# Optimization experiments

Hardware: AMD Instinct MI355X
Metric: run time of the kernel (lower is better)

Reference implementation:

```python
import jax, jax.numpy as jnp
import numpy as np

B, S, E, HEADS, LATENT = 8, 4096, 2048, 16, 64
HEAD_SIZE = E // HEADS  # 128
NEG = -1e20


def setup_inputs() -> dict:
    key = jax.random.key(0)
    k0, k1, k2, k3, k4 = jax.random.split(key, 5)
    return {
        "x": jax.random.normal(k0, (B, S, E), dtype=jnp.float32) * 0.02,
        "W_dkv": jax.random.normal(k1, (LATENT, E), dtype=jnp.float32) * 0.02,
        "W_k": jax.random.normal(k2, (HEAD_SIZE, LATENT), dtype=jnp.float32) * 0.02,
        "W_v": jax.random.normal(k3, (HEAD_SIZE, LATENT), dtype=jnp.float32) * 0.02,
        "W_q": jax.random.normal(k4, (HEAD_SIZE, E), dtype=jnp.float32) * 0.02,
    }


def reference(x, W_dkv, W_k, W_v, W_q):
    # x: [B,S,E]; nn.Linear computes x @ W.T (weight layout [out,in])
    head_size = W_k.shape[0]
    latent = jnp.einsum("bse,le->bsl", x, W_dkv)        # latent KV cache [B,S,L]
    absorbed_q = W_q.T @ W_k                              # [E,H] @ [H,L] -> [E,L]
    q_res = jnp.einsum("bse,el->bsl", x, absorbed_q)     # [B,S,L]
    scale = head_size ** -0.5
    scores = jnp.einsum("bql,bkl->bqk", q_res, latent) * scale  # [B,S,S]
    seq = x.shape[1]
    causal = jnp.tril(jnp.ones((seq, seq), dtype=bool))
    scores = jnp.where(causal, scores, NEG)
    attn = jax.nn.softmax(scores, axis=-1)               # dropout skipped (eval mode)
    v = jnp.einsum("bsl,hl->bsh", latent, W_v)           # compressed V [B,S,H]
    out = jnp.einsum("bqk,bkh->bqh", attn, v)            # [B,S,head_size]
    return out, latent  # latent == kv_cache returned by the module
```

## Files before the change

kernel.cpp:

```cpp
#include <hip/hip_runtime.h>
#include <hip/hip_bf16.h>

#define NB 8
#define NS 4096
#define NE 2048
#define NL 64
#define NH 128
#define NM (NB*NS)

typedef unsigned short ushort_t;
typedef __attribute__((ext_vector_type(4))) float f32x4;
typedef __attribute__((ext_vector_type(8))) __bf16 bf16x8;
typedef __attribute__((ext_vector_type(8))) unsigned short u16x8;
typedef __attribute__((ext_vector_type(4))) unsigned short u16x4;

#define SCALE2 0.1275174537f

__device__ __forceinline__ float fast_exp2(float x) {
    return __builtin_amdgcn_exp2f(x);
}

__device__ __forceinline__ unsigned short f2bf(float f) {
    union { float f; unsigned u; } v; v.f = f;
    unsigned u = v.u + 0x7fffu + ((v.u >> 16) & 1u);
    return (unsigned short)(u >> 16);
}

__device__ __forceinline__ float bf2f(ushort_t u) {
    union { unsigned u; float f; } v; v.u = (unsigned)u << 16; return v.f;
}

__device__ __forceinline__ int swz(int row, int colbyte) {
    return (row * 128 + colbyte) ^ ((row & 7) << 4);
}

__device__ __forceinline__ void wg_barrier() {
    asm volatile("s_waitcnt lgkmcnt(0)" ::: "memory");
    __builtin_amdgcn_s_barrier();
    __builtin_amdgcn_sched_barrier(0);
}

__global__ __launch_bounds__(256) void prep_kernel(
    const float* __restrict__ Wdkv, const float* __restrict__ Wk,
    const float* __restrict__ Wq, ushort_t* __restrict__ WcatT)
{
    __shared__ float wk[128 * 64];
    const int t = threadIdx.x;
    for (int i = t; i < 128 * 64; i += 256) wk[i] = Wk[i];
    __syncthreads();
    const int e = blockIdx.x * 256 + t;
    const int l0 = blockIdx.y * 16;
    float acc[16];
    #pragma unroll
    for (int l = 0; l < 16; ++l) acc[l] = 0.f;
    for (int h = 0; h < 128; ++h) {
        float q = Wq[h * NE + e];
        #pragma unroll
        for (int l = 0; l < 16; ++l) acc[l] += q * wk[h * 64 + l0 + l];
    }
    for (int l = 0; l < 16; ++l) WcatT[(64 + l0 + l) * NE + e] = f2bf(acc[l] * SCALE2);
    for (int l = 0; l < 16; ++l) WcatT[(l0 + l) * NE + e] = f2bf(Wdkv[(l0 + l) * NE + e]);
}

__global__ __launch_bounds__(256) void proj_kernel(
    const float* __restrict__ x, const ushort_t* __restrict__ WcatT,
    float* __restrict__ latent_out, ushort_t* __restrict__ k_bf,
    ushort_t* __restrict__ q_bf, ushort_t* __restrict__ kt)
{
    __shared__ ushort_t As[2][64 * 64];
    __shared__ ushort_t Bs[2][128 * 64];
    const int tid = threadIdx.x;
    const int w = tid >> 6, lane = tid & 63, lg = lane >> 4, li = lane & 15;
    const int m0 = blockIdx.x * 64;
    const int wm = (w >> 1) * 32, wn = (w & 1) * 64;
    const int srow = tid >> 3, scol = tid & 7;

    f32x4 acc[2][4];
    #pragma unroll
    for (int i = 0; i < 2; ++i)
        #pragma unroll
        for (int j = 0; j < 4; ++j) acc[i][j] = f32x4{0.f, 0.f, 0.f, 0.f};

    f32x4 a0reg[2][2], a1reg[2][2];
    u16x8 b0reg[4], b1reg[4];

#define PLOAD(k0, AR, BR) do { \
    _Pragma("unroll") for (int p = 0; p < 2; ++p) { \
        const float* gp = x + (long)(m0 + srow + 32 * p) * NE + (k0) + scol * 8; \
        AR[p][0] = *reinterpret_cast<const f32x4*>(gp); \
        AR[p][1] = *reinterpret_cast<const f32x4*>(gp + 4); } \
    _Pragma("unroll") for (int p = 0; p < 4; ++p) \
        BR[p] = *reinterpret_cast<const u16x8*>(WcatT + (long)(srow + 32 * p) * NE + (k0) + scol * 8); \
} while (0)

#define PWRITE(AR, BR, buf) do { \
    _Pragma("unroll") for (int p = 0; p < 2; ++p) { \
        union { unsigned uw[4]; u16x8 v; } hu; \
        asm("v_cvt_pk_bf16_f32 %0, %1, %2" : "=v"(hu.uw[0]) : "v"(AR[p][0][0]), "v"(AR[p][0][1])); \
        asm("v_cvt_pk_bf16_f32 %0, %1, %2" : "=v"(hu.uw[1]) : "v"(AR[p][0][2]), "v"(AR[p][0][3])); \
        asm("v_cvt_pk_bf16_f32 %0, %1, %2" : "=v"(hu.uw[2]) : "v"(AR[p][1][0]), "v"(AR[p][1][1])); \
        asm("v_cvt_pk_bf16_f32 %0, %1, %2" : "=v"(hu.uw[3]) : "v"(AR[p][1][2]), "v"(AR[p][1][3])); \
        *reinterpret_cast<u16x8*>(reinterpret_cast<char*>(As[buf]) + swz(srow + 32 * p, scol * 16)) = hu.v; } \
    _Pragma("unroll") for (int p = 0; p < 4; ++p) \
        *reinterpret_cast<u16x8*>(reinterpret_cast<char*>(Bs[buf]) + swz(srow + 32 * p, scol * 16)) = BR[p]; \
} while (0)

    auto compute = [&](int buf) {
        #pragma unroll
        for (int c = 0; c < 2; ++c) {
            bf16x8 af[2], bfv[4];
            #pragma unroll
            for (int mf = 0; mf < 2; ++mf)
                af[mf] = *reinterpret_cast<const bf16x8*>(
                    reinterpret_cast<const char*>(As[buf]) + swz(wm + 16 * mf + li, c * 64 + lg * 16));
            #pragma unroll
            for (int nf = 0; nf < 4; ++nf)
                bfv[nf] = *reinterpret_cast<const bf16x8*>(
                    reinterpret_cast<const char*>(Bs[buf]) + swz(wn + 16 * nf + li, c * 64 + lg * 16));
            #pragma unroll
            for (int mf = 0; mf < 2; ++mf)
                #pragma unroll
                for (int nf = 0; nf < 4; ++nf)
                    acc[mf][nf] = __builtin_amdgcn_mfma_f32_16x16x32_bf16(
                        af[mf], bfv[nf], acc[mf][nf], 0, 0, 0);
        }
    };

    PLOAD(0, a0reg, b0reg);
    PLOAD(64, a1reg, b1reg);
    PWRITE(a0reg, b0reg, 0);
    wg_barrier();

    for (int ks = 0; ks < 32; ks += 2) {
        if (ks + 2 < 32) PLOAD((ks + 2) * 64, a0reg, b0reg);
        compute(0);
        PWRITE(a1reg, b1reg, 1);
        wg_barrier();
        if (ks + 3 < 32) PLOAD((ks + 3) * 64, a1reg, b1reg);
        compute(1);
        if (ks + 2 < 32) PWRITE(a0reg, b0reg, 0);
        wg_barrier();
    }

    const int b = m0 >> 12, s0 = m0 & 4095;
    #pragma unroll
    for (int mf = 0; mf < 2; ++mf) {
        #pragma unroll
        for (int nf = 0; nf < 4; ++nf) {
            int col = wn + 16 * nf + li;
            #pragma unroll
            for (int r = 0; r < 4; ++r) {
                int row = m0 + wm + 16 * mf + 4 * lg + r;
                float v = acc[mf][nf][r];
                if (wn == 0) {
                    latent_out[(long)row * NL + col] = v;
                    k_bf[(long)row * NL + col] = f2bf(v);
                    *reinterpret_cast<ushort_t*>(reinterpret_cast<char*>(As[0]) +
                        swz(wm + 16 * mf + 4 * lg + r, col * 2)) = f2bf(v);
                } else {
                    q_bf[(long)row * NL + (col - 64)] = f2bf(v);
                }
            }
        }
    }
    wg_barrier();
    union { u16x8 u; bf16x8 v; } iu;
    #pragma unroll
    for (int j = 0; j < 8; ++j)
        iu.u[j] = (lg == (li >> 3) + 2 * (w & 1) && (li & 7) == j)
                      ? (ushort_t)0x3F80 : (ushort_t)0;
    const int ckt = w >> 1;
    f32x4 ktacc[4];
    #pragma unroll
    for (int nf = 0; nf < 4; ++nf) {
        bf16x8 bfv = *reinterpret_cast<const bf16x8*>(
            reinterpret_cast<const char*>(As[0]) + swz(16 * nf + li, ckt * 64 + lg * 16));
        ktacc[nf] = __builtin_amdgcn_mfma_f32_16x16x32_bf16(
            iu.v, bfv, f32x4{0.f, 0.f, 0.f, 0.f}, 0, 0, 0);
    }
    #pragma unroll
    for (int nf = 0; nf < 4; ++nf)
        #pragma unroll
        for (int r = 0; r < 4; ++r)
            kt[(long)(b * 64 + 16 * w + 4 * lg + r) * NS + s0 + 16 * nf + li] =
                f2bf(ktacc[nf][r]);
}

__global__ __launch_bounds__(256, 2) void attn_kernel(
    const ushort_t* __restrict__ q_bf, const ushort_t* __restrict__ k_bf,
    const ushort_t* __restrict__ kt, const float* __restrict__ Wv,
    float* __restrict__ out)
{
    __shared__ __attribute__((aligned(16))) char smem[34816];
    ushort_t* OW = (ushort_t*)smem;
    float* mw = (float*)(smem + 32768);
    float* lw = (float*)(smem + 33792);
    ushort_t* Ms = (ushort_t*)smem;
    ushort_t* Wvs = (ushort_t*)(smem + 8192);
    float* Os = (float*)smem;

    const int tid = threadIdx.x;
    const int w = tid >> 6, lane = tid & 63, lg = lane >> 4, li = lane & 15;
    const int l = blockIdx.x;
    const int b = l & 7;
    const int p_ = l >> 3;
    const int k_ = p_ >> 1, e_ = p_ & 1, kk = (k_ & 15) * 2;
    const int qt = (k_ >> 4) ? (e_ ? kk + 1 : 63 - kk) : (e_ ? 62 - kk : kk);
    const int Q0 = qt << 6;
    const int nch = (qt >> 1) + 1;

    const int krow = tid >> 1, khalf = tid & 1;
    const int trow = tid >> 2, tkq = (tid & 3) * 32;

    bf16x8 qf[4][2];
    #pragma unroll
    for (int qb = 0; qb < 4; ++qb)
        #pragma unroll
        for (int c = 0; c < 2; ++c)
            qf[qb][c] = *reinterpret_cast<const bf16x8*>(
                q_bf + ((long)b * NS + Q0 + 16 * qb + li) * NL + c * 32 + lg * 8);

    float m_r[4], l_r[4];
    #pragma unroll
    for (int qb = 0; qb < 4; ++qb) { m_r[qb] = -1.0e30f; l_r[qb] = 0.f; }
    f32x4 oacc[4][4];
    #pragma unroll
    for (int qb = 0; qb < 4; ++qb)
        #pragma unroll
        for (int n = 0; n < 4; ++n) oacc[qb][n] = f32x4{0.f, 0.f, 0.f, 0.f};

    u16x8 kreg[4], treg[4];

#define ALOAD(ch) do { \
    const int kv0_ = (ch) * 128; \
    _Pragma("unroll") for (int pp = 0; pp < 4; ++pp) \
        kreg[pp] = *reinterpret_cast<const u16x8*>( \
            k_bf + ((long)b * NS + kv0_ + krow) * NL + khalf * 32 + pp * 8); \
    _Pragma("unroll") for (int pp = 0; pp < 4; ++pp) \
        treg[pp] = *reinterpret_cast<const u16x8*>( \
            kt + ((long)b * 64 + trow) * NS + kv0_ + tkq + pp * 8); \
} while (0)

#define AWRITE() do { \
    char* Kb_ = smem; \
    char* Tb_ = smem + 16384; \
    _Pragma("unroll") for (int pp = 0; pp < 4; ++pp) \
        *reinterpret_cast<u16x8*>(Kb_ + swz(krow, khalf * 64 + pp * 16)) = kreg[pp]; \
    _Pragma("unroll") for (int pp = 0; pp < 4; ++pp) { \
        const int kv8 = tkq + pp * 8; \
        const int colp = (kv8 & 0x60) | ((kv8 & 0xC) << 1) | ((kv8 & 0x10) >> 2); \
        const int xo = (trow & 15) << 4; \
        u16x4 lo = {treg[pp][0], treg[pp][1], treg[pp][2], treg[pp][3]}; \
        u16x4 hi = {treg[pp][4], treg[pp][5], treg[pp][6], treg[pp][7]}; \
        *reinterpret_cast<u16x4*>(Tb_ + trow * 256 + ((colp * 2) ^ xo)) = lo; \
        *reinterpret_cast<u16x4*>(Tb_ + trow * 256 + (((colp + 8) * 2) ^ xo)) = hi; \
    } \
} while (0)

    auto compute = [&](bool diag, int kv0) {
        const char* Kb = smem;
        const char* Tb = smem + 16384;
        f32x4 s[2][4];
        #pragma unroll
        for (int kvb = 0; kvb < 2; ++kvb)
            #pragma unroll
            for (int qb = 0; qb < 4; ++qb) s[kvb][qb] = f32x4{0.f, 0.f, 0.f, 0.f};
        __builtin_amdgcn_s_setprio(1);
        #pragma unroll
        for (int c = 0; c < 2; ++c)
            #pragma unroll
            for (int kvb = 0; kvb < 2; ++kvb) {
                bf16x8 a = *reinterpret_cast<const bf16x8*>(
                    Kb + swz(32 * w + 16 * kvb + li, c * 64 + lg * 16));
                #pragma unroll
                for (int qb = 0; qb < 4; ++qb)
                    s[kvb][qb] = __builtin_amdgcn_mfma_f32_16x16x32_bf16(
                        a, qf[qb][c], s[kvb][qb], 0, 0, 0);
            }
        __builtin_amdgcn_s_setprio(0);
        if (diag) {
            #pragma unroll
            for (int kvb = 0; kvb < 2; ++kvb)
                #pragma unroll
                for (int qb = 0; qb < 4; ++qb)
                    #pragma unroll
                    for (int r = 0; r < 4; ++r) {
                        int kv_g = kv0 + 32 * w + 16 * kvb + 4 * lg + r;
                        int q_g = Q0 + 16 * qb + li;
                        if (kv_g > q_g) s[kvb][qb][r] = -3.0e38f;
                    }
        }
        float mx[4];
        #pragma unroll
        for (int qb = 0; qb < 4; ++qb) {
            float m0_ = fmaxf(fmaxf(s[0][qb][0], s[0][qb][1]), fmaxf(s[0][qb][2], s[0][qb][3]));
            float m1_ = fmaxf(fmaxf(s[1][qb][0], s[1][qb][1]), fmaxf(s[1][qb][2], s[1][qb][3]));
            mx[qb] = fmaxf(m0_, m1_);
        }
        bool ok = (mx[0] <= m_r[0] + 8.f) && (mx[1] <= m_r[1] + 8.f) &&
                  (mx[2] <= m_r[2] + 8.f) && (mx[3] <= m_r[3] + 8.f);
        if (!__all(ok)) {
            #pragma unroll
            for (int qb = 0; qb < 4; ++qb) {
                float mxf = fmaxf(mx[qb], __shfl_xor(mx[qb], 16));
                mxf = fmaxf(mxf, __shfl_xor(mxf, 32));
                float m_new = fmaxf(m_r[qb], mxf);
                float corr = fast_exp2(m_r[qb] - m_new);
                m_r[qb] = m_new;
                l_r[qb] *= corr;
                float corrO[4];
                #pragma unroll
                for (int r = 0; r < 4; ++r)
                    corrO[r] = __shfl(corr, (lane & 48) | (4 * lg + r));
                #pragma unroll
                for (int n = 0; n < 4; ++n)
                    #pragma unroll
                    for (int r = 0; r < 4; ++r) oacc[qb][n][r] *= corrO[r];
            }
        }
        #pragma unroll
        for (int qb = 0; qb < 4; ++qb) {
            float rs = 0.f;
            #pragma unroll
            for (int kvb = 0; kvb < 2; ++kvb)
                #pragma unroll
                for (int r = 0; r < 4; ++r) {
                    float pv = fast_exp2(s[kvb][qb][r] - m_r[qb]);
                    s[kvb][qb][r] = pv;
                    rs += pv;
                }
            l_r[qb] += rs;
        }
        bf16x8 vb[4];
        #pragma unroll
        for (int n = 0; n < 4; ++n)
            vb[n] = *reinterpret_cast<const bf16x8*>(
                Tb + (16 * n + li) * 256 + ((64 * w + 16 * lg) ^ (li << 4)));
        __builtin_amdgcn_s_setprio(1);
        #pragma unroll
        for (int qb = 0; qb < 4; ++qb) {
            union { unsigned uw[4]; bf16x8 v; } pa;
            asm("v_cvt_pk_bf16_f32 %0, %1, %2" : "=v"(pa.uw[0]) : "v"(s[0][qb][0]), "v"(s[0][qb][1]));
            asm("v_cvt_pk_bf16_f32 %0, %1, %2" : "=v"(pa.uw[1]) : "v"(s[0][qb][2]), "v"(s[0][qb][3]));
            asm("v_cvt_pk_bf16_f32 %0, %1, %2" : "=v"(pa.uw[2]) : "v"(s[1][qb][0]), "v"(s[1][qb][1]));
            asm("v_cvt_pk_bf16_f32 %0, %1, %2" : "=v"(pa.uw[3]) : "v"(s[1][qb][2]), "v"(s[1][qb][3]));
            #pragma unroll
            for (int n = 0; n < 4; ++n)
                oacc[qb][n] = __builtin_amdgcn_mfma_f32_16x16x32_bf16(
                    pa.v, vb[n], oacc[qb][n], 0, 0, 0);
        }
        __builtin_amdgcn_s_setprio(0);
    };

    ALOAD(0);
    AWRITE();
    wg_barrier();
    for (int i = 0; i < nch; ++i) {
        if (i + 1 < nch) ALOAD(i + 1);
        compute(i == nch - 1, i * 128);
        wg_barrier();
        if (i + 1 < nch) {
            AWRITE();
            wg_barrier();
        }
    }

    #pragma unroll
    for (int qb = 0; qb < 4; ++qb) {
        l_r[qb] += __shfl_xor(l_r[qb], 16);
        l_r[qb] += __shfl_xor(l_r[qb], 32);
    }
    if (lg == 0) {
        #pragma unroll
        for (int qb = 0; qb < 4; ++qb) {
            mw[w * 64 + 16 * qb + li] = m_r[qb];
            lw[w * 64 + 16 * qb + li] = l_r[qb];
        }
    }
    #pragma unroll
    for (int qb = 0; qb < 4; ++qb)
        #pragma unroll
        for (int r = 0; r < 4; ++r) {
            union { unsigned uw[2]; u16x4 v; } u;
            asm("v_cvt_pk_bf16_f32 %0, %1, %2" : "=v"(u.uw[0]) : "v"(oacc[qb][0][r]), "v"(oacc[qb][1][r]));
            asm("v_cvt_pk_bf16_f32 %0, %1, %2" : "=v"(u.uw[1]) : "v"(oacc[qb][2][r]), "v"(oacc[qb][3][r]));
            int q = 16 * qb + 4 * lg + r;
            *reinterpret_cast<u16x4*>(OW + (w * 64 + q) * 64 + li * 4) = u.v;
        }
    wg_barrier();

    float merged[16];
    {
        const int q = tid >> 2, g = tid & 3;
        float m4[4], l4[4];
        #pragma unroll
        for (int ww = 0; ww < 4; ++ww) { m4[ww] = mw[ww * 64 + q]; l4[ww] = lw[ww * 64 + q]; }
        float M = fmaxf(fmaxf(m4[0], m4[1]), fmaxf(m4[2], m4[3]));
        float cw[4], L = 0.f;
        #pragma unroll
        for (int ww = 0; ww < 4; ++ww) { cw[ww] = fast_exp2(m4[ww] - M); L += cw[ww] * l4[ww]; }
        float inv = 1.f / L;
        #pragma unroll
        for (int e = 0; e < 16; ++e) {
            float a = 0.f;
            #pragma unroll
            for (int ww = 0; ww < 4; ++ww)
                a += cw[ww] * bf2f(OW[(ww * 64 + q) * 64 + e * 4 + g]);
            merged[e] = a * inv;
        }
    }
    wg_barrier();

    {
        const int q = tid >> 2, g = tid & 3;
        #pragma unroll
        for (int ee = 0; ee < 8; ++ee) {
            unsigned pk;
            asm("v_cvt_pk_bf16_f32 %0, %1, %2" : "=v"(pk) : "v"(merged[2 * ee]), "v"(merged[2 * ee + 1]));
            *reinterpret_cast<unsigned*>(reinterpret_cast<char*>(Ms) + swz(q, g * 32 + 4 * ee)) = pk;
        }
        const int r = tid >> 1, hf = tid & 1;
        const float* wp = Wv + r * 64 + hf * 32;
        #pragma unroll
        for (int qq = 0; qq < 2; ++qq) {
            f32x4 w0 = *reinterpret_cast<const f32x4*>(wp + qq * 16);
            f32x4 w1 = *reinterpret_cast<const f32x4*>(wp + qq * 16 + 4);
            f32x4 w2 = *reinterpret_cast<const f32x4*>(wp + qq * 16 + 8);
            f32x4 w3 = *reinterpret_cast<const f32x4*>(wp + qq * 16 + 12);
            u16x8 h0, h1;
            #pragma unroll
            for (int jj = 0; jj < 4; ++jj) {
                h0[jj] = f2bf(w0[jj]); h0[4 + jj] = f2bf(w1[jj]);
                h1[jj] = f2bf(w2[jj]); h1[4 + jj] = f2bf(w3[jj]);
            }
            *reinterpret_cast<u16x8*>(reinterpret_cast<char*>(Wvs) + swz(r, hf * 64 + qq * 32)) = h0;
            *reinterpret_cast<u16x8*>(reinterpret_cast<char*>(Wvs) + swz(r, hf * 64 + qq * 32 + 16)) = h1;
        }
    }
    wg_barrier();

    f32x4 vacc[2][4];
    #pragma unroll
    for (int i = 0; i < 2; ++i)
        #pragma unroll
        for (int j = 0; j < 4; ++j) vacc[i][j] = f32x4{0.f, 0.f, 0.f, 0.f};
    #pragma unroll
    for (int c = 0; c < 2; ++c) {
        bf16x8 af[2], bfv[4];
        #pragma unroll
        for (int mf = 0; mf < 2; ++mf)
            af[mf] = *reinterpret_cast<const bf16x8*>(
                reinterpret_cast<const char*>(Wvs) + swz(32 * w + 16 * mf + li, c * 64 + lg * 16));
        #pragma unroll
        for (int nf = 0; nf < 4; ++nf)
            bfv[nf] = *reinterpret_cast<const bf16x8*>(
                reinterpret_cast<const char*>(Ms) + swz(16 * nf + li, c * 64 + lg * 16));
        #pragma unroll
        for (int mf = 0; mf < 2; ++mf)
            #pragma unroll
            for (int nf = 0; nf < 4; ++nf)
                vacc[mf][nf] = __builtin_amdgcn_mfma_f32_16x16x32_bf16(
                    af[mf], bfv[nf], vacc[mf][nf], 0, 0, 0);
    }
    wg_barrier();
    #pragma unroll
    for (int mf = 0; mf < 2; ++mf)
        #pragma unroll
        for (int nf = 0; nf < 4; ++nf)
            #pragma unroll
            for (int r = 0; r < 4; ++r)
                Os[(16 * nf + li) * 132 + 32 * w + 16 * mf + 4 * lg + r] = vacc[mf][nf][r];
    wg_barrier();
    {
        const int r = tid >> 2, cb = (tid & 3) * 32;
        float* op = out + ((long)b * NS + Q0 + r) * NH + cb;
        const float* sp = Os + r * 132 + cb;
        #pragma unroll
        for (int qq = 0; qq < 8; ++qq)
            *reinterpret_cast<f32x4*>(op + 4 * qq) = *reinterpret_cast<const f32x4*>(sp + 4 * qq);
    }
}

extern "C" void kernel_launch(void* const* d_in, const int* in_sizes, int n_in,
                              void* d_out, int out_size, void* d_ws, size_t ws_size,
                              hipStream_t stream) {
    const float* x    = (const float*)d_in[0];
    const float* Wdkv = (const float*)d_in[1];
    const float* Wk   = (const float*)d_in[2];
    const float* Wv   = (const float*)d_in[3];
    const float* Wq   = (const float*)d_in[4];

    float* out = (float*)d_out;
    float* latent_out = out + (long)NM * NH;

    ushort_t* WcatT = (ushort_t*)d_ws;
    ushort_t* q_bf  = WcatT + 128 * NE;
    ushort_t* k_bf  = q_bf + (long)NM * NL;
    ushort_t* kt    = k_bf + (long)NM * NL;

    hipLaunchKernelGGL(prep_kernel, dim3(NE / 256, 4), dim3(256), 0, stream, Wdkv, Wk, Wq, WcatT);
    hipLaunchKernelGGL(proj_kernel, dim3(NM / 64), dim3(256), 0, stream,
                       x, WcatT, latent_out, k_bf, q_bf, kt);
    hipLaunchKernelGGL(attn_kernel, dim3(512), dim3(256), 0, stream,
                       q_bf, k_bf, kt, Wv, out);
}
```

Before: 131.8 us.

## Halve attention query tile to 32 rows and double the grid

The attention kernel now processes 32 query rows per workgroup instead of 64 and launches 1024 workgroups instead of 512, with a new causal tile ordering that pairs short and long tiles. The aim is better CU occupancy and load balance on the 256-CU part, along with lower register pressure per block. The cross-wave merge is rewritten to use 8 threads per query row, a swizzled bf16 shared-memory layout and vectorized reads. In exchange, K/V tiles are reloaded from global/L2 twice as often per query, and each MFMA now has less reuse of the loaded K data.

```diff
diff --git a/kernel.cpp b/kernel.cpp
--- a/kernel.cpp
+++ b/kernel.cpp
@@ -194,38 +194,38 @@
     __shared__ __attribute__((aligned(16))) char smem[34816];
     ushort_t* OW = (ushort_t*)smem;
     float* mw = (float*)(smem + 32768);
-    float* lw = (float*)(smem + 33792);
+    float* lw = (float*)(smem + 33280);
     ushort_t* Ms = (ushort_t*)smem;
-    ushort_t* Wvs = (ushort_t*)(smem + 8192);
+    ushort_t* Wvs = (ushort_t*)(smem + 4096);
     float* Os = (float*)smem;
 
     const int tid = threadIdx.x;
     const int w = tid >> 6, lane = tid & 63, lg = lane >> 4, li = lane & 15;
-    const int l = blockIdx.x;
-    const int b = l & 7;
-    const int p_ = l >> 3;
-    const int k_ = p_ >> 1, e_ = p_ & 1, kk = (k_ & 15) * 2;
-    const int qt = (k_ >> 4) ? (e_ ? kk + 1 : 63 - kk) : (e_ ? 62 - kk : kk);
-    const int Q0 = qt << 6;
-    const int nch = (qt >> 1) + 1;
+    const int j = blockIdx.x;
+    const int b = j & 7;
+    const int s_ = j >> 3;
+    const int u_ = s_ & 63, e_ = s_ >> 6;
+    const int t = e_ ? u_ : 127 - u_;
+    const int Q0 = t << 5;
+    const int nch = (t >> 2) + 1;
 
     const int krow = tid >> 1, khalf = tid & 1;
     const int trow = tid >> 2, tkq = (tid & 3) * 32;
 
-    bf16x8 qf[4][2];
-    #pragma unroll
-    for (int qb = 0; qb < 4; ++qb)
+    bf16x8 qf[2][2];
+    #pragma unroll
+    for (int qb = 0; qb < 2; ++qb)
         #pragma unroll
         for (int c = 0; c < 2; ++c)
             qf[qb][c] = *reinterpret_cast<const bf16x8*>(
                 q_bf + ((long)b * NS + Q0 + 16 * qb + li) * NL + c * 32 + lg * 8);
 
-    float m_r[4], l_r[4];
-    #pragma unroll
-    for (int qb = 0; qb < 4; ++qb) { m_r[qb] = -1.0e30f; l_r[qb] = 0.f; }
-    f32x4 oacc[4][4];
-    #pragma unroll
-    for (int qb = 0; qb < 4; ++qb)
+    float m_r[2], l_r[2];
+    m_r[0] = m_r[1] = -1.0e30f;
+    l_r[0] = l_r[1] = 0.f;
+    f32x4 oacc[2][4];
+    #pragma unroll
+    for (int qb = 0; qb < 2; ++qb)
         #pragma unroll
         for (int n = 0; n < 4; ++n) oacc[qb][n] = f32x4{0.f, 0.f, 0.f, 0.f};
 
@@ -260,11 +260,11 @@
     auto compute = [&](bool diag, int kv0) {
         const char* Kb = smem;
         const char* Tb = smem + 16384;
-        f32x4 s[2][4];
+        f32x4 s[2][2];
         #pragma unroll
         for (int kvb = 0; kvb < 2; ++kvb)
             #pragma unroll
-            for (int qb = 0; qb < 4; ++qb) s[kvb][qb] = f32x4{0.f, 0.f, 0.f, 0.f};
+            for (int qb = 0; qb < 2; ++qb) s[kvb][qb] = f32x4{0.f, 0.f, 0.f, 0.f};
         __builtin_amdgcn_s_setprio(1);
         #pragma unroll
         for (int c = 0; c < 2; ++c)
@@ -273,7 +273,7 @@
                 bf16x8 a = *reinterpret_cast<const bf16x8*>(
                     Kb + swz(32 * w + 16 * kvb + li, c * 64 + lg * 16));
                 #pragma unroll
-                for (int qb = 0; qb < 4; ++qb)
+                for (int qb = 0; qb < 2; ++qb)
                     s[kvb][qb] = __builtin_amdgcn_mfma_f32_16x16x32_bf16(
                         a, qf[qb][c], s[kvb][qb], 0, 0, 0);
             }
@@ -282,7 +282,7 @@
             #pragma unroll
             for (int kvb = 0; kvb < 2; ++kvb)
                 #pragma unroll
-                for (int qb = 0; qb < 4; ++qb)
+                for (int qb = 0; qb < 2; ++qb)
                     #pragma unroll
                     for (int r = 0; r < 4; ++r) {
                         int kv_g = kv0 + 32 * w + 16 * kvb + 4 * lg + r;
@@ -290,18 +290,17 @@
                         if (kv_g > q_g) s[kvb][qb][r] = -3.0e38f;
                     }
         }
-        float mx[4];
-        #pragma unroll
-        for (int qb = 0; qb < 4; ++qb) {
+        float mx[2];
+        #pragma unroll
+        for (int qb = 0; qb < 2; ++qb) {
             float m0_ = fmaxf(fmaxf(s[0][qb][0], s[0][qb][1]), fmaxf(s[0][qb][2], s[0][qb][3]));
             float m1_ = fmaxf(fmaxf(s[1][qb][0], s[1][qb][1]), fmaxf(s[1][qb][2], s[1][qb][3]));
             mx[qb] = fmaxf(m0_, m1_);
         }
-        bool ok = (mx[0] <= m_r[0] + 8.f) && (mx[1] <= m_r[1] + 8.f) &&
-                  (mx[2] <= m_r[2] + 8.f) && (mx[3] <= m_r[3] + 8.f);
+        bool ok = (mx[0] <= m_r[0] + 8.f) && (mx[1] <= m_r[1] + 8.f);
         if (!__all(ok)) {
             #pragma unroll
-            for (int qb = 0; qb < 4; ++qb) {
+            for (int qb = 0; qb < 2; ++qb) {
                 float mxf = fmaxf(mx[qb], __shfl_xor(mx[qb], 16));
                 mxf = fmaxf(mxf, __shfl_xor(mxf, 32));
                 float m_new = fmaxf(m_r[qb], mxf);
@@ -319,7 +318,7 @@
             }
         }
         #pragma unroll
-        for (int qb = 0; qb < 4; ++qb) {
+        for (int qb = 0; qb < 2; ++qb) {
             float rs = 0.f;
             #pragma unroll
             for (int kvb = 0; kvb < 2; ++kvb)
@@ -338,7 +337,7 @@
                 Tb + (16 * n + li) * 256 + ((64 * w + 16 * lg) ^ (li << 4)));
         __builtin_amdgcn_s_setprio(1);
         #pragma unroll
-        for (int qb = 0; qb < 4; ++qb) {
+        for (int qb = 0; qb < 2; ++qb) {
             union { unsigned uw[4]; bf16x8 v; } pa;
             asm("v_cvt_pk_bf16_f32 %0, %1, %2" : "=v"(pa.uw[0]) : "v"(s[0][qb][0]), "v"(s[0][qb][1]));
             asm("v_cvt_pk_bf16_f32 %0, %1, %2" : "=v"(pa.uw[1]) : "v"(s[0][qb][2]), "v"(s[0][qb][3]));
@@ -366,58 +365,60 @@
     }
 
     #pragma unroll
-    for (int qb = 0; qb < 4; ++qb) {
+    for (int qb = 0; qb < 2; ++qb) {
         l_r[qb] += __shfl_xor(l_r[qb], 16);
         l_r[qb] += __shfl_xor(l_r[qb], 32);
     }
     if (lg == 0) {
         #pragma unroll
-        for (int qb = 0; qb < 4; ++qb) {
-            mw[w * 64 + 16 * qb + li] = m_r[qb];
-            lw[w * 64 + 16 * qb + li] = l_r[qb];
-        }
-    }
-    #pragma unroll
-    for (int qb = 0; qb < 4; ++qb)
+        for (int qb = 0; qb < 2; ++qb) {
+            mw[w * 32 + 16 * qb + li] = m_r[qb];
+            lw[w * 32 + 16 * qb + li] = l_r[qb];
+        }
+    }
+    #pragma unroll
+    for (int qb = 0; qb < 2; ++qb)
         #pragma unroll
         for (int r = 0; r < 4; ++r) {
             union { unsigned uw[2]; u16x4 v; } u;
             asm("v_cvt_pk_bf16_f32 %0, %1, %2" : "=v"(u.uw[0]) : "v"(oacc[qb][0][r]), "v"(oacc[qb][1][r]));
             asm("v_cvt_pk_bf16_f32 %0, %1, %2" : "=v"(u.uw[1]) : "v"(oacc[qb][2][r]), "v"(oacc[qb][3][r]));
             int q = 16 * qb + 4 * lg + r;
-            *reinterpret_cast<u16x4*>(OW + (w * 64 + q) * 64 + li * 4) = u.v;
-        }
-    wg_barrier();
-
-    float merged[16];
+            *reinterpret_cast<u16x4*>(smem + (w * 32 + q) * 128 + ((li * 8) ^ ((q & 7) << 4))) = u.v;
+        }
+    wg_barrier();
+
+    float acc8[8];
     {
-        const int q = tid >> 2, g = tid & 3;
+        const int q2 = tid >> 3, g = tid & 7;
         float m4[4], l4[4];
         #pragma unroll
-        for (int ww = 0; ww < 4; ++ww) { m4[ww] = mw[ww * 64 + q]; l4[ww] = lw[ww * 64 + q]; }
+        for (int ww = 0; ww < 4; ++ww) { m4[ww] = mw[ww * 32 + q2]; l4[ww] = lw[ww * 32 + q2]; }
         float M = fmaxf(fmaxf(m4[0], m4[1]), fmaxf(m4[2], m4[3]));
-        float cw[4], L = 0.f;
-        #pragma unroll
-        for (int ww = 0; ww < 4; ++ww) { cw[ww] = fast_exp2(m4[ww] - M); L += cw[ww] * l4[ww]; }
+        float a4[4], L = 0.f;
+        #pragma unroll
+        for (int ww = 0; ww < 4; ++ww) { a4[ww] = fast_exp2(m4[ww] - M); L += a4[ww] * l4[ww]; }
         float inv = 1.f / L;
         #pragma unroll
-        for (int e = 0; e < 16; ++e) {
-            float a = 0.f;
-            #pragma unroll
-            for (int ww = 0; ww < 4; ++ww)
-                a += cw[ww] * bf2f(OW[(ww * 64 + q) * 64 + e * 4 + g]);
-            merged[e] = a * inv;
+        for (int ww = 0; ww < 4; ++ww) a4[ww] *= inv;
+        #pragma unroll
+        for (int k = 0; k < 8; ++k) acc8[k] = 0.f;
+        const int slot = 16 * (g ^ (q2 & 7));
+        #pragma unroll
+        for (int ww = 0; ww < 4; ++ww) {
+            u16x8 v = *reinterpret_cast<const u16x8*>(smem + (ww * 32 + q2) * 128 + slot);
+            #pragma unroll
+            for (int k = 0; k < 8; ++k) acc8[k] += a4[ww] * bf2f(v[k]);
         }
     }
     wg_barrier();
 
     {
-        const int q = tid >> 2, g = tid & 3;
-        #pragma unroll
-        for (int ee = 0; ee < 8; ++ee) {
-            unsigned pk;
-            asm("v_cvt_pk_bf16_f32 %0, %1, %2" : "=v"(pk) : "v"(merged[2 * ee]), "v"(merged[2 * ee + 1]));
-            *reinterpret_cast<unsigned*>(reinterpret_cast<char*>(Ms) + swz(q, g * 32 + 4 * ee)) = pk;
+        const int q2 = tid >> 3, g = tid & 7;
+        #pragma unroll
+        for (int k = 0; k < 8; ++k) {
+            int dv = 16 * (k & 3) + 2 * g + (k >> 2);
+            *reinterpret_cast<ushort_t*>(reinterpret_cast<char*>(Ms) + swz(q2, dv * 2)) = f2bf(acc8[k]);
         }
         const int r = tid >> 1, hf = tid & 1;
         const float* wp = Wv + r * 64 + hf * 32;
@@ -439,26 +440,26 @@
     }
     wg_barrier();
 
-    f32x4 vacc[2][4];
+    f32x4 vacc[2][2];
     #pragma unroll
     for (int i = 0; i < 2; ++i)
         #pragma unroll
-        for (int j = 0; j < 4; ++j) vacc[i][j] = f32x4{0.f, 0.f, 0.f, 0.f};
+        for (int jj = 0; jj < 2; ++jj) vacc[i][jj] = f32x4{0.f, 0.f, 0.f, 0.f};
     #pragma unroll
     for (int c = 0; c < 2; ++c) {
-        bf16x8 af[2], bfv[4];
+        bf16x8 af[2], bfv[2];
         #pragma unroll
         for (int mf = 0; mf < 2; ++mf)
             af[mf] = *reinterpret_cast<const bf16x8*>(
                 reinterpret_cast<const char*>(Wvs) + swz(32 * w + 16 * mf + li, c * 64 + lg * 16));
         #pragma unroll
-        for (int nf = 0; nf < 4; ++nf)
+        for (int nf = 0; nf < 2; ++nf)
             bfv[nf] = *reinterpret_cast<const bf16x8*>(
                 reinterpret_cast<const char*>(Ms) + swz(16 * nf + li, c * 64 + lg * 16));
         #pragma unroll
         for (int mf = 0; mf < 2; ++mf)
             #pragma unroll
-            for (int nf = 0; nf < 4; ++nf)
+            for (int nf = 0; nf < 2; ++nf)
                 vacc[mf][nf] = __builtin_amdgcn_mfma_f32_16x16x32_bf16(
                     af[mf], bfv[nf], vacc[mf][nf], 0, 0, 0);
     }
@@ -466,17 +467,17 @@
     #pragma unroll
     for (int mf = 0; mf < 2; ++mf)
         #pragma unroll
-        for (int nf = 0; nf < 4; ++nf)
+        for (int nf = 0; nf < 2; ++nf)
             #pragma unroll
             for (int r = 0; r < 4; ++r)
                 Os[(16 * nf + li) * 132 + 32 * w + 16 * mf + 4 * lg + r] = vacc[mf][nf][r];
     wg_barrier();
     {
-        const int r = tid >> 2, cb = (tid & 3) * 32;
+        const int r = tid >> 3, cb = (tid & 7) * 16;
         float* op = out + ((long)b * NS + Q0 + r) * NH + cb;
         const float* sp = Os + r * 132 + cb;
         #pragma unroll
-        for (int qq = 0; qq < 8; ++qq)
+        for (int qq = 0; qq < 4; ++qq)
             *reinterpret_cast<f32x4*>(op + 4 * qq) = *reinterpret_cast<const f32x4*>(sp + 4 * qq);
     }
 }
@@ -501,6 +502,6 @@
     hipLaunchKernelGGL(prep_kernel, dim3(NE / 256, 4), dim3(256), 0, stream, Wdkv, Wk, Wq, WcatT);
     hipLaunchKernelGGL(proj_kernel, dim3(NM / 64), dim3(256), 0, stream,
                        x, WcatT, latent_out, k_bf, q_bf, kt);
-    hipLaunchKernelGGL(attn_kernel, dim3(512), dim3(256), 0, stream,
+    hipLaunchKernelGGL(attn_kernel, dim3(1024), dim3(256), 0, stream,
                        q_bf, k_bf, kt, Wv, out);
 }
```

Measured after the change: 137.3 us. 4.2% more time.
